# Optimization experiments

Hardware: AMD Instinct MI355X
Metric: run time of the kernel (lower is better)

Reference implementation:

```python
import jax, jax.numpy as jnp
import numpy as np

GRID = 3
K = GRID ** 3          # keypoints per proposal (grid rep)
RADIUS = 0.2
NSAMPLE = 16


def _rotz(t):
    c, s = jnp.cos(t), jnp.sin(t)
    z, o = jnp.zeros_like(t), jnp.ones_like(t)
    return jnp.stack([jnp.stack([c, -s, z], -1),
                      jnp.stack([s,  c, z], -1),
                      jnp.stack([z,  z, o], -1)], -2)  # [..., 3, 3]


def _grid_keypoints(boxes, origins, heading):
    # boxes: [B,P,6] = (left,back,down,right,front,up) absolute distances from origin
    B, P, _ = boxes.shape
    ii = jnp.stack(jnp.meshgrid(jnp.arange(GRID), jnp.arange(GRID), jnp.arange(GRID), indexing='ij'), -1)
    dense = ii.reshape(K, 3).astype(boxes.dtype)  # same order as ones(g,g,g).nonzero()
    size = boxes[..., 0:3] + boxes[..., 3:6]                       # [B,P,3]
    local = (dense + 0.5) / GRID * size[:, :, None, :] - boxes[..., None, 0:3]  # [B,P,K,3]
    R = _rotz(heading)                                             # [B,P,3,3]
    pts = jnp.einsum('bpkc,bpcd->bpkd', local, R) + origins[:, :, None, :]
    return pts.reshape(B, P * K, 3)


def _ball_query(key_pts, seed_xyz):
    # key_pts [B,M,3], seed_xyz [B,N,3] -> neighbor indices [B,M,NSAMPLE]
    N = seed_xyz.shape[1]
    d2 = (jnp.sum(key_pts ** 2, -1)[:, :, None]
          + jnp.sum(seed_xyz ** 2, -1)[:, None, :]
          - 2.0 * jnp.einsum('bmc,bnc->bmn', key_pts, seed_xyz))   # [B,M,N]
    cand = jnp.where(d2 < RADIUS ** 2, jnp.arange(N, dtype=jnp.int32), N)
    idx = -jax.lax.top_k(-cand, NSAMPLE)[0]  # first NSAMPLE in-radius indices, ascending
    first = idx[..., 0:1]
    fill = jnp.where(first == N, 0, first)   # empty ball -> index 0 (CUDA kernel default)
    return jnp.where(idx == N, fill, idx)


def _forward(seed_xyz, seed_features, boxes, origins, heading, W1, b1, W2, b2, W3, b3, Wr, br):
    B, P = boxes.shape[:2]
    key_pts = _grid_keypoints(boxes, origins, heading)             # [B,M,3], M=P*K
    idx = _ball_query(key_pts, seed_xyz)                           # [B,M,S]
    b_idx = jnp.arange(B)[:, None, None]
    gx = seed_xyz[b_idx, idx]                                      # [B,M,S,3]
    gf = jnp.transpose(seed_features, (0, 2, 1))[b_idx, idx]       # [B,M,S,C]
    gxyz = (gx - key_pts[:, :, None, :]) / RADIUS                  # normalize_xyz=True
    x = jnp.concatenate([gxyz, gf], -1)                            # use_xyz: [B,M,S,3+C]
    x = jax.nn.relu(x @ W1 + b1)                                   # shared per-point MLP
    x = jax.nn.relu(x @ W2 + b2)
    x = jax.nn.relu(x @ W3 + b3)
    x = jnp.max(x, axis=2)                                         # max-pool over ball -> [B,M,32]
    f = x.reshape(B, P, K, 32)
    # original: [B,32,M] -> view(B,32,P,K) -> transpose(2,3) -> reshape(B,32*K,P)
    f = jnp.transpose(f, (0, 1, 3, 2)).reshape(B, P, 32 * K)       # channel-major (c*K+k) layout
    out = f @ Wr.T + br                                            # 1x1 conv reduce -> [B,P,128]
    return jnp.transpose(out, (0, 2, 1))                           # [B,128,P]


def setup_inputs() -> dict:
    key = jax.random.key(0)
    ks = jax.random.split(key, 9)
    B, N, C, P = 2, 1024, 256, 256
    return {
        'seed_xyz': jax.random.normal(ks[0], (B, N, 3), jnp.float32),
        'seed_features': jax.random.normal(ks[1], (B, C, N), jnp.float32),
        'boxes': jax.random.uniform(ks[2], (B, P, 6), jnp.float32, 0.1, 1.0),
        'origins': jax.random.normal(ks[3], (B, P, 3), jnp.float32),
        'heading': jax.random.uniform(ks[4], (B, P), jnp.float32, 0.0, 6.2831853),
        'W1': jax.random.normal(ks[5], (C + 3, 128), jnp.float32) * 0.05,
        'b1': jnp.zeros((128,), jnp.float32),
        'W2': jax.random.normal(ks[6], (128, 64), jnp.float32) * 0.05,
        'b2': jnp.zeros((64,), jnp.float32),
        'W3': jax.random.normal(ks[7], (64, 32), jnp.float32) * 0.05,
        'b3': jnp.zeros((32,), jnp.float32),
        'Wr': jax.random.normal(ks[8], (128, 32 * K), jnp.float32) * 0.05,
        'br': jnp.zeros((128,), jnp.float32),
    }


def reference(seed_xyz, seed_features, boxes, origins, heading, W1, b1, W2, b2, W3, b3, Wr, br):
    return _forward(seed_xyz, seed_features, boxes, origins, heading, W1, b1, W2, b2, W3, b3, Wr, br)
```

## Files before the change

### kernel.cpp

```cpp
#include <hip/hip_runtime.h>

#define B_ 2
#define N_ 1024
#define C_ 256
#define P_ 256
#define K_ 27
#define M_ (P_ * K_)
#define TOTKP (B_ * M_)
#define NS 16
#define R2C 0.04f
#define QDIM 864


#define PREP_WRT0    256
#define PREP_BALLQ0  364
#define PREP_NBLK    3820

__global__ __launch_bounds__(256) void prep_k(
    const float* __restrict__ sf, const float* __restrict__ W1,
    const float* __restrict__ b1, const float* __restrict__ Wr,
    const float* __restrict__ seed_xyz, const float* __restrict__ boxes,
    const float* __restrict__ origins, const float* __restrict__ heading,
    float* __restrict__ F, float* __restrict__ WrT,
    float4* __restrict__ kp4, int* __restrict__ cntw, int* __restrict__ idxw)
{
    __shared__ __align__(16) float ssf[C_ * 8];
    int tid = threadIdx.x;
    int bid = blockIdx.x;

    if (bid < PREP_WRT0) {
        int b = bid >> 7;
        int n0 = (bid & 127) * 8;
        for (int e = tid; e < C_ * 8; e += 256) {
            int c = e >> 3, i = e & 7;
            ssf[e] = sf[(b * C_ + c) * N_ + n0 + i];
        }
        __syncthreads();
        int j = tid & 127;
        int h = tid >> 7;
        float acc[4];
        float bj = b1[j];
#pragma unroll
        for (int i = 0; i < 4; i++) acc[i] = bj;
#pragma unroll 8
        for (int c = 0; c < C_; ++c) {
            float w = W1[(3 + c) * 128 + j];
            float4 s = *(const float4*)&ssf[c * 8 + h * 4];
            acc[0] = fmaf(s.x, w, acc[0]);
            acc[1] = fmaf(s.y, w, acc[1]);
            acc[2] = fmaf(s.z, w, acc[2]);
            acc[3] = fmaf(s.w, w, acc[3]);
        }
#pragma unroll
        for (int i = 0; i < 4; i++)
            F[(b * N_ + n0 + h * 4 + i) * 128 + j] = acc[i];
    } else if (bid < PREP_BALLQ0) {
        int e4 = (bid - PREP_WRT0) * 256 + tid;
        int j = e4 / 216, qq = e4 - j * 216;
        float4 v = ((const float4*)(Wr + j * QDIM))[qq];
        int q0 = qq * 4;
        WrT[(q0 + 0) * 128 + j] = v.x;
        WrT[(q0 + 1) * 128 + j] = v.y;
        WrT[(q0 + 2) * 128 + j] = v.z;
        WrT[(q0 + 3) * 128 + j] = v.w;
    } else {
        int wid = tid >> 6, lane = tid & 63;
        int kpg = (bid - PREP_BALLQ0) * 4 + wid;
        int b = kpg / M_;
        int m = kpg - b * M_;
        int p = m / K_, a = m - p * K_;

        const float* bx = boxes + (b * P_ + p) * 6;
        const float* og = origins + (b * P_ + p) * 3;
        float th = heading[b * P_ + p];
        float di = (float)(a / 9), dj = (float)((a / 3) % 3), dk = (float)(a % 3);
        float s0 = __fadd_rn(bx[0], bx[3]);
        float s1 = __fadd_rn(bx[1], bx[4]);
        float s2 = __fadd_rn(bx[2], bx[5]);
        float lx = __fsub_rn(__fmul_rn(__fdiv_rn(__fadd_rn(di, 0.5f), 3.0f), s0), bx[0]);
        float ly = __fsub_rn(__fmul_rn(__fdiv_rn(__fadd_rn(dj, 0.5f), 3.0f), s1), bx[1]);
        float lz = __fsub_rn(__fmul_rn(__fdiv_rn(__fadd_rn(dk, 0.5f), 3.0f), s2), bx[2]);
        float ct = cosf(th), st = sinf(th);
        float kx = __fadd_rn(__fadd_rn(__fmul_rn(lx, ct), __fmul_rn(ly, st)), og[0]);
        float ky = __fadd_rn(__fadd_rn(__fmul_rn(lx, -st), __fmul_rn(ly, ct)), og[1]);
        float kz = __fadd_rn(lz, og[2]);
        if (lane == 0) kp4[kpg] = make_float4(kx, ky, kz, 0.f);
        float kk = __fadd_rn(__fadd_rn(__fmul_rn(kx, kx), __fmul_rn(ky, ky)),
                             __fmul_rn(kz, kz));

        const float* sb = seed_xyz + b * (N_ * 3) + lane * 48;
        float f[48];
#pragma unroll
        for (int q = 0; q < 12; q++)
            ((float4*)f)[q] = ((const float4*)sb)[q];

        unsigned mask = 0;
#pragma unroll
        for (int i = 0; i < 16; i++) {
            float x = f[3 * i], y = f[3 * i + 1], z = f[3 * i + 2];
            float ss = __fadd_rn(__fadd_rn(__fmul_rn(x, x), __fmul_rn(y, y)),
                                 __fmul_rn(z, z));
            float dot = __fadd_rn(__fadd_rn(__fmul_rn(kx, x), __fmul_rn(ky, y)),
                                  __fmul_rn(kz, z));
            float d2 = __fsub_rn(__fadd_rn(kk, ss), __fmul_rn(2.0f, dot));
            mask |= (d2 < R2C ? 1u : 0u) << i;
        }

        int pc = __popc(mask);
        int incl = pc;
#pragma unroll
        for (int d = 1; d < 64; d <<= 1) {
            int v = __shfl_up(incl, d);
            if (lane >= d) incl += v;
        }
        int total = __shfl(incl, 63);
        int base = incl - pc;

        int* ip = idxw + kpg * NS;
        unsigned mm = mask;
        while (mm && base < NS) {
            int i = __ffs(mm) - 1;
            mm &= mm - 1;
            ip[base++] = lane * 16 + i;
        }
        if (lane == 0) cntw[kpg] = total < NS ? total : NS;
    }
}

struct Ctx {
    const float* seed; const float* F;
    const float* sW2; const float* sW3;
    float* sH1; float* sH2;
    const int* ip;
    float4 kp;
    float w1x0, w1y0, w1z0, w1x1, w1y1, w1z1, b2j, b3t;
    int lane, t, jh, b, cnt, n0;
};

template <int GS>
static __device__ __forceinline__ void do_group(const Ctx& c, int s0, float& pool)
{
    float gx[GS], gy[GS], gz[GS];
    int nn[GS];
#pragma unroll
    for (int u = 0; u < GS; u++) {
        int s = s0 + u;
        int n = (s < c.cnt) ? c.ip[s] : c.n0;
        nn[u] = n;
        const float* sp = c.seed + (c.b * N_ + n) * 3;
        gx[u] = __fdiv_rn(__fsub_rn(sp[0], c.kp.x), 0.2f);
        gy[u] = __fdiv_rn(__fsub_rn(sp[1], c.kp.y), 0.2f);
        gz[u] = __fdiv_rn(__fsub_rn(sp[2], c.kp.z), 0.2f);
    }
#pragma unroll
    for (int u = 0; u < GS; u++) {
        const float* fp = c.F + (c.b * N_ + nn[u]) * 128;
        float v0 = fp[c.lane];
        float v1 = fp[c.lane + 64];
        v0 = fmaf(gx[u], c.w1x0, fmaf(gy[u], c.w1y0, fmaf(gz[u], c.w1z0, v0)));
        v1 = fmaf(gx[u], c.w1x1, fmaf(gy[u], c.w1y1, fmaf(gz[u], c.w1z1, v1)));
        c.sH1[u * 128 + c.lane] = fmaxf(v0, 0.f);
        c.sH1[u * 128 + c.lane + 64] = fmaxf(v1, 0.f);
    }
    float acc[GS];
#pragma unroll
    for (int u = 0; u < GS; u++) acc[u] = c.b2j;
#pragma unroll
    for (int cc = 0; cc < 128; cc += 4) {
        float w0 = c.sW2[(cc + 0) * 64 + c.lane];
        float w1 = c.sW2[(cc + 1) * 64 + c.lane];
        float w2 = c.sW2[(cc + 2) * 64 + c.lane];
        float w3 = c.sW2[(cc + 3) * 64 + c.lane];
#pragma unroll
        for (int u = 0; u < GS; u++) {
            float4 h = *(const float4*)&c.sH1[u * 128 + cc];
            acc[u] = fmaf(h.x, w0, fmaf(h.y, w1, fmaf(h.z, w2, fmaf(h.w, w3, acc[u]))));
        }
    }
#pragma unroll
    for (int u = 0; u < GS; u++) c.sH2[u * 64 + c.lane] = fmaxf(acc[u], 0.f);
    float a3[GS];
#pragma unroll
    for (int u = 0; u < GS; u++) a3[u] = (c.jh == 0) ? c.b3t : 0.f;
#pragma unroll
    for (int jj = 0; jj < 32; jj += 4) {
        int j0 = c.jh * 32 + jj;
        float w0 = c.sW3[(j0 + 0) * 32 + c.t];
        float w1 = c.sW3[(j0 + 1) * 32 + c.t];
        float w2 = c.sW3[(j0 + 2) * 32 + c.t];
        float w3 = c.sW3[(j0 + 3) * 32 + c.t];
#pragma unroll
        for (int u = 0; u < GS; u++) {
            float4 h = *(const float4*)&c.sH2[u * 64 + j0];
            a3[u] = fmaf(h.x, w0, fmaf(h.y, w1, fmaf(h.z, w2, fmaf(h.w, w3, a3[u]))));
        }
    }
#pragma unroll
    for (int u = 0; u < GS; u++) {
        float v = a3[u] + __shfl_xor(a3[u], 32);
        pool = fmaxf(pool, fmaxf(v, 0.f));
    }
}

__global__ __launch_bounds__(256, 2) void pf_k(
    const float* __restrict__ seed_xyz, const float* __restrict__ F,
    const float* __restrict__ W1, const float* __restrict__ b2g,
    const float* __restrict__ b3g, const float* __restrict__ W2g,
    const float* __restrict__ W3g, const float* __restrict__ WrT,
    const float* __restrict__ br, const float4* __restrict__ kp4,
    const int* __restrict__ cntw, const int* __restrict__ idxw,
    float* __restrict__ out)
{
    __shared__ __align__(16) float sW2[128 * 64];
    __shared__ __align__(16) float sW3[64 * 32];
    __shared__ __align__(16) float sH1[4 * 4 * 128];
    __shared__ __align__(16) float sH2[4 * 4 * 64];
    __shared__ __align__(16) float ft[QDIM];
    __shared__ __align__(16) float pj[128];
    int tid = threadIdx.x;
    for (int e = tid; e < 2048; e += 256)
        ((float4*)sW2)[e] = ((const float4*)W2g)[e];
    for (int e = tid; e < 512; e += 256)
        ((float4*)sW3)[e] = ((const float4*)W3g)[e];

    int wid = tid >> 6, lane = tid & 63;
    int bp = blockIdx.x;
    int b = bp >> 8, p = bp & 255;

    Ctx c;
    c.seed = seed_xyz; c.F = F;
    c.sW2 = sW2; c.sW3 = sW3;
    c.sH1 = sH1 + wid * 4 * 128;
    c.sH2 = sH2 + wid * 4 * 64;
    c.lane = lane; c.t = lane & 31; c.jh = lane >> 5;
    c.b = b;
    c.w1x0 = W1[lane];       c.w1x1 = W1[lane + 64];
    c.w1y0 = W1[128 + lane]; c.w1y1 = W1[128 + lane + 64];
    c.w1z0 = W1[256 + lane]; c.w1z1 = W1[256 + lane + 64];
    c.b2j = b2g[lane]; c.b3t = b3g[lane & 31];
    __syncthreads();

    for (int k = wid; k < K_; k += 4) {
        int kpg = bp * K_ + k;
        c.kp = kp4[kpg];
        c.cnt = cntw[kpg];
        c.ip = idxw + kpg * NS;
        c.n0 = (c.cnt > 0) ? c.ip[0] : 0;
        int scnt = c.cnt < 1 ? 1 : c.cnt;
        float pool = 0.f;
        for (int s0 = 0; s0 < scnt; s0 += 4) {
            int gs = scnt - s0; gs = gs > 4 ? 4 : gs;
            switch (gs) {
                case 1: do_group<1>(c, s0, pool); break;
                case 2: do_group<2>(c, s0, pool); break;
                case 3: do_group<3>(c, s0, pool); break;
                default: do_group<4>(c, s0, pool); break;
            }
        }
        if (lane < 32) ft[lane * K_ + k] = pool;
    }
    __syncthreads();

    int j = tid & 127;
    int h = tid >> 7;
    float a = 0.f;
    const float* fq = ft + h * 432;
    const float* wq = WrT + (h * 432) * 128 + j;
#pragma unroll 4
    for (int q = 0; q < 432; ++q)
        a = fmaf(fq[q], wq[q * 128], a);
    if (h == 1) pj[j] = a;
    __syncthreads();
    if (h == 0)
        out[(b * 128 + j) * 256 + p] = a + pj[j] + br[j];
}

extern "C" void kernel_launch(void* const* d_in, const int* in_sizes, int n_in,
                              void* d_out, int out_size, void* d_ws, size_t ws_size,
                              hipStream_t stream)
{
    const float* seed_xyz  = (const float*)d_in[0];
    const float* seed_feat = (const float*)d_in[1];
    const float* boxes     = (const float*)d_in[2];
    const float* origins   = (const float*)d_in[3];
    const float* heading   = (const float*)d_in[4];
    const float* W1        = (const float*)d_in[5];
    const float* b1        = (const float*)d_in[6];
    const float* W2        = (const float*)d_in[7];
    const float* b2        = (const float*)d_in[8];
    const float* W3        = (const float*)d_in[9];
    const float* b3        = (const float*)d_in[10];
    const float* Wr        = (const float*)d_in[11];
    const float* br        = (const float*)d_in[12];
    float* out = (float*)d_out;

    char* ws = (char*)d_ws;
    float4* kp4  = (float4*)(ws);
    int*    cntw = (int*)(ws + 221184);
    int*    idxw = (int*)(ws + 276480);
    float*  F    = (float*)(ws + 1161216);
    float*  WrT  = (float*)(ws + 2209792);

    prep_k<<<dim3(PREP_NBLK), dim3(256), 0, stream>>>(
        seed_feat, W1, b1, Wr, seed_xyz, boxes, origins, heading,
        F, WrT, kp4, cntw, idxw);
    pf_k<<<dim3(512), dim3(256), 0, stream>>>(
        seed_xyz, F, W1, b2, b3, W2, W3, WrT, br, kp4, cntw, idxw, out);
}
```

Before: 148.5 us.

## Flatten per-block neighbor samples into a packed work list and pool with atomicMax

The per-keypoint loop, where each of 4 warps walked whole keypoints with variable sample counts, is replaced. A block-level prefix scan now packs all (keypoint, neighbor) pairs into a shared work list. Eight warps take groups of 4 samples from that list, which balances the uneven ball-query counts. Max-pooling now uses shared-memory integer atomicMax on non-negative float bits, and the final projection is split across 4 partial sums. This costs extra block setup, syncs and atomics, and asks for 512-thread blocks with higher occupancy bounds, which may pressure registers.

After: 160.0 us. +7.8%, slower.

```diff
diff --git a/kernel.cpp b/kernel.cpp
--- a/kernel.cpp
+++ b/kernel.cpp
@@ -127,82 +127,7 @@
     }
 }
 
-struct Ctx {
-    const float* seed; const float* F;
-    const float* sW2; const float* sW3;
-    float* sH1; float* sH2;
-    const int* ip;
-    float4 kp;
-    float w1x0, w1y0, w1z0, w1x1, w1y1, w1z1, b2j, b3t;
-    int lane, t, jh, b, cnt, n0;
-};
-
-template <int GS>
-static __device__ __forceinline__ void do_group(const Ctx& c, int s0, float& pool)
-{
-    float gx[GS], gy[GS], gz[GS];
-    int nn[GS];
-#pragma unroll
-    for (int u = 0; u < GS; u++) {
-        int s = s0 + u;
-        int n = (s < c.cnt) ? c.ip[s] : c.n0;
-        nn[u] = n;
-        const float* sp = c.seed + (c.b * N_ + n) * 3;
-        gx[u] = __fdiv_rn(__fsub_rn(sp[0], c.kp.x), 0.2f);
-        gy[u] = __fdiv_rn(__fsub_rn(sp[1], c.kp.y), 0.2f);
-        gz[u] = __fdiv_rn(__fsub_rn(sp[2], c.kp.z), 0.2f);
-    }
-#pragma unroll
-    for (int u = 0; u < GS; u++) {
-        const float* fp = c.F + (c.b * N_ + nn[u]) * 128;
-        float v0 = fp[c.lane];
-        float v1 = fp[c.lane + 64];
-        v0 = fmaf(gx[u], c.w1x0, fmaf(gy[u], c.w1y0, fmaf(gz[u], c.w1z0, v0)));
-        v1 = fmaf(gx[u], c.w1x1, fmaf(gy[u], c.w1y1, fmaf(gz[u], c.w1z1, v1)));
-        c.sH1[u * 128 + c.lane] = fmaxf(v0, 0.f);
-        c.sH1[u * 128 + c.lane + 64] = fmaxf(v1, 0.f);
-    }
-    float acc[GS];
-#pragma unroll
-    for (int u = 0; u < GS; u++) acc[u] = c.b2j;
-#pragma unroll
-    for (int cc = 0; cc < 128; cc += 4) {
-        float w0 = c.sW2[(cc + 0) * 64 + c.lane];
-        float w1 = c.sW2[(cc + 1) * 64 + c.lane];
-        float w2 = c.sW2[(cc + 2) * 64 + c.lane];
-        float w3 = c.sW2[(cc + 3) * 64 + c.lane];
-#pragma unroll
-        for (int u = 0; u < GS; u++) {
-            float4 h = *(const float4*)&c.sH1[u * 128 + cc];
-            acc[u] = fmaf(h.x, w0, fmaf(h.y, w1, fmaf(h.z, w2, fmaf(h.w, w3, acc[u]))));
-        }
-    }
-#pragma unroll
-    for (int u = 0; u < GS; u++) c.sH2[u * 64 + c.lane] = fmaxf(acc[u], 0.f);
-    float a3[GS];
-#pragma unroll
-    for (int u = 0; u < GS; u++) a3[u] = (c.jh == 0) ? c.b3t : 0.f;
-#pragma unroll
-    for (int jj = 0; jj < 32; jj += 4) {
-        int j0 = c.jh * 32 + jj;
-        float w0 = c.sW3[(j0 + 0) * 32 + c.t];
-        float w1 = c.sW3[(j0 + 1) * 32 + c.t];
-        float w2 = c.sW3[(j0 + 2) * 32 + c.t];
-        float w3 = c.sW3[(j0 + 3) * 32 + c.t];
-#pragma unroll
-        for (int u = 0; u < GS; u++) {
-            float4 h = *(const float4*)&c.sH2[u * 64 + j0];
-            a3[u] = fmaf(h.x, w0, fmaf(h.y, w1, fmaf(h.z, w2, fmaf(h.w, w3, a3[u]))));
-        }
-    }
-#pragma unroll
-    for (int u = 0; u < GS; u++) {
-        float v = a3[u] + __shfl_xor(a3[u], 32);
-        pool = fmaxf(pool, fmaxf(v, 0.f));
-    }
-}
-
-__global__ __launch_bounds__(256, 2) void pf_k(
+__global__ __launch_bounds__(512, 4) void pf_k(
     const float* __restrict__ seed_xyz, const float* __restrict__ F,
     const float* __restrict__ W1, const float* __restrict__ b2g,
     const float* __restrict__ b3g, const float* __restrict__ W2g,
@@ -213,66 +138,153 @@
 {
     __shared__ __align__(16) float sW2[128 * 64];
     __shared__ __align__(16) float sW3[64 * 32];
-    __shared__ __align__(16) float sH1[4 * 4 * 128];
-    __shared__ __align__(16) float sH2[4 * 4 * 64];
-    __shared__ __align__(16) float ft[QDIM];
-    __shared__ __align__(16) float pj[128];
+    __shared__ __align__(16) float sH1[8 * 4 * 128];
+    __shared__ __align__(16) float sH2[8 * 4 * 64];
+    __shared__ __align__(16) int   ft_i[QDIM];
+    __shared__ __align__(16) int   swl[K_ * NS];
+    __shared__ __align__(16) float4 skp[K_];
+    __shared__ int scnt[K_], koff[K_], sS;
+    __shared__ __align__(16) float spart[512];
+
     int tid = threadIdx.x;
-    for (int e = tid; e < 2048; e += 256)
-        ((float4*)sW2)[e] = ((const float4*)W2g)[e];
-    for (int e = tid; e < 512; e += 256)
-        ((float4*)sW3)[e] = ((const float4*)W3g)[e];
-
     int wid = tid >> 6, lane = tid & 63;
     int bp = blockIdx.x;
     int b = bp >> 8, p = bp & 255;
 
-    Ctx c;
-    c.seed = seed_xyz; c.F = F;
-    c.sW2 = sW2; c.sW3 = sW3;
-    c.sH1 = sH1 + wid * 4 * 128;
-    c.sH2 = sH2 + wid * 4 * 64;
-    c.lane = lane; c.t = lane & 31; c.jh = lane >> 5;
-    c.b = b;
-    c.w1x0 = W1[lane];       c.w1x1 = W1[lane + 64];
-    c.w1y0 = W1[128 + lane]; c.w1y1 = W1[128 + lane + 64];
-    c.w1z0 = W1[256 + lane]; c.w1z1 = W1[256 + lane + 64];
-    c.b2j = b2g[lane]; c.b3t = b3g[lane & 31];
-    __syncthreads();
-
-    for (int k = wid; k < K_; k += 4) {
-        int kpg = bp * K_ + k;
-        c.kp = kp4[kpg];
-        c.cnt = cntw[kpg];
-        c.ip = idxw + kpg * NS;
-        c.n0 = (c.cnt > 0) ? c.ip[0] : 0;
-        int scnt = c.cnt < 1 ? 1 : c.cnt;
-        float pool = 0.f;
-        for (int s0 = 0; s0 < scnt; s0 += 4) {
-            int gs = scnt - s0; gs = gs > 4 ? 4 : gs;
-            switch (gs) {
-                case 1: do_group<1>(c, s0, pool); break;
-                case 2: do_group<2>(c, s0, pool); break;
-                case 3: do_group<3>(c, s0, pool); break;
-                default: do_group<4>(c, s0, pool); break;
+    for (int e = tid; e < 2048; e += 512)
+        ((float4*)sW2)[e] = ((const float4*)W2g)[e];
+    for (int e = tid; e < 512; e += 512)
+        ((float4*)sW3)[e] = ((const float4*)W3g)[e];
+    for (int e = tid; e < QDIM; e += 512)
+        ft_i[e] = 0;
+    if (tid < K_) {
+        int kpg = bp * K_ + tid;
+        scnt[tid] = cntw[kpg];
+        skp[tid] = kp4[kpg];
+    }
+    __syncthreads();
+
+    if (wid == 0) {
+        int lc = 0;
+        if (lane < K_) {
+            int cc = scnt[lane];
+            lc = cc > 0 ? cc : 1;
+        }
+        int incl = lc;
+#pragma unroll
+        for (int d = 1; d < 32; d <<= 1) {
+            int v = __shfl_up(incl, d);
+            if (lane >= d) incl += v;
+        }
+        if (lane < K_) koff[lane] = incl - lc;
+        if (lane == K_ - 1) sS = incl;
+    }
+    __syncthreads();
+
+    if (tid < K_ * NS) {
+        int k = tid >> 4, s = tid & 15;
+        int cc = scnt[k];
+        int lc = cc > 0 ? cc : 1;
+        if (s < lc) {
+            int n = (s < cc) ? idxw[(bp * K_ + k) * NS + s] : 0;
+            swl[koff[k] + s] = (k << 16) | n;
+        }
+    }
+    __syncthreads();
+
+    int S = sS;
+    int G = (S + 3) >> 2;
+
+    float w1x0 = W1[lane],        w1x1 = W1[lane + 64];
+    float w1y0 = W1[128 + lane],  w1y1 = W1[128 + lane + 64];
+    float w1z0 = W1[256 + lane],  w1z1 = W1[256 + lane + 64];
+    float b2j = b2g[lane];
+    float b3t = b3g[lane & 31];
+    int jh = lane >> 5;
+    int t = lane & 31;
+    float* myH1 = sH1 + wid * 4 * 128;
+    float* myH2 = sH2 + wid * 4 * 64;
+
+    for (int g = wid; g < G; g += 8) {
+        int kk4[4], nn[4];
+        float gx[4], gy[4], gz[4];
+#pragma unroll
+        for (int u = 0; u < 4; u++) {
+            int e = 4 * g + u; if (e >= S) e = S - 1;
+            int w = swl[e];
+            int k = w >> 16, n = w & 0xffff;
+            kk4[u] = k; nn[u] = n;
+            float4 kp = skp[k];
+            const float* sp = seed_xyz + (b * N_ + n) * 3;
+            gx[u] = __fdiv_rn(__fsub_rn(sp[0], kp.x), 0.2f);
+            gy[u] = __fdiv_rn(__fsub_rn(sp[1], kp.y), 0.2f);
+            gz[u] = __fdiv_rn(__fsub_rn(sp[2], kp.z), 0.2f);
+        }
+#pragma unroll
+        for (int u = 0; u < 4; u++) {
+            const float* fp = F + (b * N_ + nn[u]) * 128;
+            float v0 = fp[lane];
+            float v1 = fp[lane + 64];
+            v0 = fmaf(gx[u], w1x0, fmaf(gy[u], w1y0, fmaf(gz[u], w1z0, v0)));
+            v1 = fmaf(gx[u], w1x1, fmaf(gy[u], w1y1, fmaf(gz[u], w1z1, v1)));
+            myH1[u * 128 + lane] = fmaxf(v0, 0.f);
+            myH1[u * 128 + lane + 64] = fmaxf(v1, 0.f);
+        }
+        float acc[4];
+#pragma unroll
+        for (int u = 0; u < 4; u++) acc[u] = b2j;
+#pragma unroll
+        for (int cc = 0; cc < 128; cc += 4) {
+            float w0 = sW2[(cc + 0) * 64 + lane];
+            float w1 = sW2[(cc + 1) * 64 + lane];
+            float w2 = sW2[(cc + 2) * 64 + lane];
+            float w3 = sW2[(cc + 3) * 64 + lane];
+#pragma unroll
+            for (int u = 0; u < 4; u++) {
+                float4 h = *(const float4*)&myH1[u * 128 + cc];
+                acc[u] = fmaf(h.x, w0, fmaf(h.y, w1, fmaf(h.z, w2, fmaf(h.w, w3, acc[u]))));
             }
         }
-        if (lane < 32) ft[lane * K_ + k] = pool;
+#pragma unroll
+        for (int u = 0; u < 4; u++) myH2[u * 64 + lane] = fmaxf(acc[u], 0.f);
+        float a3[4];
+#pragma unroll
+        for (int u = 0; u < 4; u++) a3[u] = (jh == 0) ? b3t : 0.f;
+#pragma unroll
+        for (int jj = 0; jj < 32; jj += 4) {
+            int j0 = jh * 32 + jj;
+            float w0 = sW3[(j0 + 0) * 32 + t];
+            float w1 = sW3[(j0 + 1) * 32 + t];
+            float w2 = sW3[(j0 + 2) * 32 + t];
+            float w3 = sW3[(j0 + 3) * 32 + t];
+#pragma unroll
+            for (int u = 0; u < 4; u++) {
+                float4 h = *(const float4*)&myH2[u * 64 + j0];
+                a3[u] = fmaf(h.x, w0, fmaf(h.y, w1, fmaf(h.z, w2, fmaf(h.w, w3, a3[u]))));
+            }
+        }
+#pragma unroll
+        for (int u = 0; u < 4; u++) {
+            float v = a3[u] + __shfl_xor(a3[u], 32);
+            int vi = __float_as_int(fmaxf(v, 0.f));
+            if (lane < 32) atomicMax(&ft_i[t * K_ + kk4[u]], vi);
+        }
     }
     __syncthreads();
 
     int j = tid & 127;
     int h = tid >> 7;
     float a = 0.f;
-    const float* fq = ft + h * 432;
-    const float* wq = WrT + (h * 432) * 128 + j;
+    const int* fq = ft_i + h * 216;
+    const float* wq = WrT + (h * 216) * 128 + j;
 #pragma unroll 4
-    for (int q = 0; q < 432; ++q)
-        a = fmaf(fq[q], wq[q * 128], a);
-    if (h == 1) pj[j] = a;
-    __syncthreads();
-    if (h == 0)
-        out[(b * 128 + j) * 256 + p] = a + pj[j] + br[j];
+    for (int q = 0; q < 216; ++q)
+        a = fmaf(__int_as_float(fq[q]), wq[q * 128], a);
+    spart[tid] = a;
+    __syncthreads();
+    if (tid < 128)
+        out[(b * 128 + tid) * 256 + p] =
+            spart[tid] + spart[128 + tid] + spart[256 + tid] + spart[384 + tid] + br[tid];
 }
 
 extern "C" void kernel_launch(void* const* d_in, const int* in_sizes, int n_in,
@@ -304,6 +316,6 @@
     prep_k<<<dim3(PREP_NBLK), dim3(256), 0, stream>>>(
         seed_feat, W1, b1, Wr, seed_xyz, boxes, origins, heading,
         F, WrT, kp4, cntw, idxw);
-    pf_k<<<dim3(512), dim3(256), 0, stream>>>(
+    pf_k<<<dim3(512), dim3(512), 0, stream>>>(
         seed_xyz, F, W1, b2, b3, W2, W3, WrT, br, kp4, cntw, idxw, out);
 }
```
